# Kernel tuning notes

Hardware: AMD Instinct MI355X
Metric: run time of the kernel (lower is better)

Reference implementation:

```python
import jax, jax.numpy as jnp
import numpy as np

H = 16            # num heads
D_NOPE = 128
D_ROPE = 64
D_V = 128
Q_LORA = 1536
KV_LORA = 512
HIDDEN = 2048
EPS = 1e-6


def rmsnorm(x, w):
    xf = x.astype(jnp.float32)
    var = jnp.mean(xf * xf, axis=-1, keepdims=True)
    return (w * (xf * jax.lax.rsqrt(var + EPS))).astype(x.dtype)


def rope_interleaved(x, cos, sin):
    # x: [B,H,S,D]; cos,sin: [S,D] -> use even-index entries as the per-pair values
    B, nH, S, D = x.shape
    cv = cos[:, 0::2].astype(jnp.float32)[None, None]  # [1,1,S,D/2]
    sv = sin[:, 0::2].astype(jnp.float32)[None, None]
    xf = x.astype(jnp.float32).reshape(B, nH, S, D // 2, 2)
    xr, xi = xf[..., 0], xf[..., 1]
    out = jnp.stack([xr * cv - xi * sv, xr * sv + xi * cv], axis=-1)
    return out.reshape(B, nH, S, D).astype(x.dtype)


def setup_inputs() -> dict:
    key = jax.random.key(0)
    ks = jax.random.split(key, 9)
    B, S = 2, 2048
    std = 0.02
    return {
        "hidden_states": jax.random.normal(ks[0], (B, S, HIDDEN), jnp.float32),
        "cos": jax.random.uniform(ks[1], (S, D_ROPE), jnp.float32),
        "sin": jax.random.uniform(ks[2], (S, D_ROPE), jnp.float32),
        "q_a_w": jax.random.normal(ks[3], (HIDDEN, Q_LORA), jnp.float32) * std,
        "q_a_ln_w": jnp.ones((Q_LORA,), jnp.float32),
        "q_b_w": jax.random.normal(ks[4], (Q_LORA, H * (D_NOPE + D_ROPE)), jnp.float32) * std,
        "kv_a_w": jax.random.normal(ks[5], (HIDDEN, KV_LORA + D_ROPE), jnp.float32) * std,
        "kv_a_ln_w": jnp.ones((KV_LORA,), jnp.float32),
        "kv_b_w": jax.random.normal(ks[6], (KV_LORA, H * (D_NOPE + D_V)), jnp.float32) * std,
        "o_w": jax.random.normal(ks[7], (H * D_V, HIDDEN), jnp.float32) * std,
    }


def reference(hidden_states, cos, sin, q_a_w, q_a_ln_w, q_b_w, kv_a_w, kv_a_ln_w, kv_b_w, o_w):
    B, S, _ = hidden_states.shape
    scale = 1.0 / np.sqrt(D_NOPE + D_ROPE)

    # Q path: low-rank down-proj, RMSNorm, up-proj
    q = rmsnorm(hidden_states @ q_a_w, q_a_ln_w) @ q_b_w
    q = q.reshape(B, S, H, D_NOPE + D_ROPE).transpose(0, 2, 1, 3)  # [B,H,S,Dq]
    q_nope, q_rope = q[..., :D_NOPE], q[..., D_NOPE:]

    # KV path: compressed kv + shared rope key
    ckv = hidden_states @ kv_a_w  # [B,S,KV_LORA+D_ROPE]
    compressed_kv, k_rope = ckv[..., :KV_LORA], ckv[..., KV_LORA:]
    k_rope = jnp.broadcast_to(k_rope[:, None], (B, H, S, D_ROPE))
    kv = rmsnorm(compressed_kv, kv_a_ln_w) @ kv_b_w
    kv = kv.reshape(B, S, H, D_NOPE + D_V).transpose(0, 2, 1, 3)  # [B,H,S,Dk+Dv]
    k_nope, value = kv[..., :D_NOPE], kv[..., D_NOPE:]

    q_rope = rope_interleaved(q_rope, cos, sin)
    k_rope = rope_interleaved(k_rope, cos, sin)

    query = jnp.concatenate([q_nope, q_rope], axis=-1)  # [B,H,S,192]
    key = jnp.concatenate([k_nope, k_rope], axis=-1)

    attn = jnp.einsum("bhqd,bhkd->bhqk", query, key) * scale
    attn = jax.nn.softmax(attn.astype(jnp.float32), axis=-1).astype(query.dtype)
    out = jnp.einsum("bhqk,bhkd->bhqd", attn, value)  # [B,H,S,Dv]
    out = out.transpose(0, 2, 1, 3).reshape(B, S, H * D_V)
    return out @ o_w
```

## Files before the change

### kernel.cpp

```cpp
#include <hip/hip_runtime.h>

typedef unsigned short u16;
typedef __bf16 bf16x8 __attribute__((ext_vector_type(8)));
typedef float f32x4 __attribute__((ext_vector_type(4)));

#define S_ 2048

__device__ __forceinline__ u16 f2bf(float f) {
  union { float f; unsigned u; } v; v.f = f;
  unsigned r = v.u + 0x7fffu + ((v.u >> 16) & 1u);
  return (u16)(r >> 16);
}
__device__ __forceinline__ float bf2f(u16 h) {
  union { unsigned u; float f; } v; v.u = ((unsigned)h) << 16;
  return v.f;
}

__device__ __forceinline__ f32x4 mfma16(bf16x8 a, bf16x8 b, f32x4 c) {
  return __builtin_amdgcn_mfma_f32_16x16x32_bf16(a, b, c, 0, 0, 0);
}

__device__ __forceinline__ void async16(const void* g, void* l) {
  __builtin_amdgcn_global_load_lds((__attribute__((address_space(1))) void*)g,
                                   (__attribute__((address_space(3))) void*)l,
                                   16, 0, 0);
}

__global__ void cast_bf_k(const float* __restrict__ in, u16* __restrict__ out, int n) {
  int i = blockIdx.x * 256 + threadIdx.x;
  if (i < n) out[i] = f2bf(in[i]);
}

__global__ void transw_k(const float* __restrict__ W, u16* __restrict__ Wt,
                         int K, int N) {
  __shared__ float tile[32][33];
  int k0 = blockIdx.x * 32, n0 = blockIdx.y * 32;
  int tx = threadIdx.x, ty = threadIdx.y;
#pragma unroll
  for (int r = 0; r < 32; r += 8) {
    int n = n0 + tx;
    tile[ty + r][tx] = (n < N) ? W[(long)(k0 + ty + r) * N + n] : 0.f;
  }
  __syncthreads();
#pragma unroll
  for (int r = 0; r < 32; r += 8) {
    Wt[(long)(n0 + ty + r) * K + k0 + tx] = f2bf(tile[tx][ty + r]);
  }
}

template <typename OUT_T, bool ROPE>
__global__ __launch_bounds__(256)
void gemm_bt_k(const u16* __restrict__ A, const u16* __restrict__ Bt,
               OUT_T* __restrict__ C, int K, int Nc, int ldc,
               const float* __restrict__ cs, const float* __restrict__ sn) {
  __shared__ __align__(16) u16 sA[128 * 32];
  __shared__ __align__(16) u16 sB[128 * 32];
  int tid = threadIdx.x;
  int lane = tid & 63, w = tid >> 6;
  int wr = w >> 1, wc = w & 1;
  int l15 = lane & 15, quad = lane >> 4;
  long tm = (long)blockIdx.y * 128;
  long tn = (long)blockIdx.x * 128;
  const u16* Ab = A + tm * K;
  const u16* Bb = Bt + tn * K;
  f32x4 acc[4][4] = {};

  for (int k0 = 0; k0 < K; k0 += 32) {
#pragma unroll
    for (int it = 0; it < 2; ++it) {
      int c = tid + it * 256;
      int row = c >> 2, kc = c & 3;
      async16(Ab + (long)row * K + k0 + kc * 8, sA + c * 8);
      async16(Bb + (long)row * K + k0 + kc * 8, sB + c * 8);
    }
    __syncthreads();
    bf16x8 af[4], bfr[4];
#pragma unroll
    for (int i = 0; i < 4; ++i)
      af[i] = *(const bf16x8*)(sA + (wr * 64 + i * 16 + l15) * 32 + quad * 8);
#pragma unroll
    for (int j = 0; j < 4; ++j)
      bfr[j] = *(const bf16x8*)(sB + (wc * 64 + j * 16 + l15) * 32 + quad * 8);
#pragma unroll
    for (int i = 0; i < 4; ++i)
#pragma unroll
      for (int j = 0; j < 4; ++j)
        acc[i][j] = mfma16(af[i], bfr[j], acc[i][j]);
    __syncthreads();
  }
#pragma unroll
  for (int i = 0; i < 4; ++i) {
#pragma unroll
    for (int j = 0; j < 4; ++j) {
      int col = (int)tn + wc * 64 + j * 16 + l15;
      if (col < Nc) {
        bool ropeT = false;
        int fi = 0;
        if constexpr (ROPE) {
          int d = col % 192;
          ropeT = (d >= 128);
          fi = (d - 128) & ~1;
        }
#pragma unroll
        for (int r = 0; r < 4; ++r) {
          long row = tm + wr * 64 + i * 16 + quad * 4 + r;
          float v = acc[i][j][r];
          if constexpr (ROPE) {
            float partner = __shfl_xor(v, 1);
            if (ropeT) {
              int si = (int)row & (S_ - 1);
              float cv = cs[si * 64 + fi], sv = sn[si * 64 + fi];
              v = (l15 & 1) ? (partner * sv + v * cv)
                            : (v * cv - partner * sv);
            }
          }
          if constexpr (sizeof(OUT_T) == 2) C[row * ldc + col] = f2bf(v);
          else                              C[row * ldc + col] = v;
        }
      }
    }
  }
}

__global__ __launch_bounds__(256)
void rmsnorm_k(const float* __restrict__ in, int ld, int N,
               const float* __restrict__ w, u16* __restrict__ out, int ldo) {
  int row = blockIdx.x;
  const float* x = in + (long)row * ld;
  float ss = 0.f;
  for (int i = threadIdx.x; i < N; i += 256) { float v = x[i]; ss += v * v; }
#pragma unroll
  for (int off = 32; off; off >>= 1) ss += __shfl_down(ss, off);
  __shared__ float red[4];
  if ((threadIdx.x & 63) == 0) red[threadIdx.x >> 6] = ss;
  __syncthreads();
  float inv = rsqrtf((red[0] + red[1] + red[2] + red[3]) / N + 1e-6f);
  u16* o = out + (long)row * ldo;
  for (int i = threadIdx.x; i < N; i += 256) o[i] = f2bf(w[i] * x[i] * inv);
}

__global__ void krope_k(const float* __restrict__ src, int ld,
                        const float* __restrict__ cs, const float* __restrict__ sn,
                        u16* __restrict__ out) {
  int idx = blockIdx.x * 256 + threadIdx.x;
  int row = idx >> 5, i = idx & 31;
  int s = row & (S_ - 1);
  float xr = src[(long)row * ld + 2 * i];
  float xi = src[(long)row * ld + 2 * i + 1];
  float cv = cs[s * 64 + 2 * i], sv = sn[s * 64 + 2 * i];
  out[(long)row * 64 + 2 * i]     = f2bf(xr * cv - xi * sv);
  out[(long)row * 64 + 2 * i + 1] = f2bf(xr * sv + xi * cv);
}

__global__ void kswz_k(const u16* __restrict__ kvb, const u16* __restrict__ kr,
                       u16* __restrict__ kswz) {
  int tile = blockIdx.x;
  int bh = tile >> 5, kt = tile & 31;
  int b = bh >> 4, h = bh & 15;
  u16* dst = kswz + (long)tile * 12288;
#pragma unroll
  for (int i = 0; i < 6; ++i) {
    int c = threadIdx.x + i * 256;
    int frag = c >> 6, lane = c & 63;
    int kg = frag / 6, db = frag % 6;
    int key = kt * 64 + kg * 16 + (lane & 15);
    int d = db * 32 + (lane >> 4) * 8;
    const u16* src;
    if (d < 128) src = kvb + ((long)(b * S_ + key)) * 4096 + h * 256 + d;
    else         src = kr  + ((long)(b * S_ + key)) * 64 + (d - 128);
    *(f32x4*)(dst + c * 8) = *(const f32x4*)src;
  }
}

__global__ void vswz2_k(const u16* __restrict__ kvb, u16* __restrict__ vswz) {
  int tile = blockIdx.x;
  int bh = tile >> 5, kt = tile & 31;
  int b = bh >> 4, h = bh & 15;
  __shared__ __align__(16) u16 t[64 * 136];
  int tid = threadIdx.x;
#pragma unroll
  for (int i = 0; i < 4; ++i) {
    int c = tid + i * 256;
    int row = c >> 4, dc = (c & 15) * 8;
    *(f32x4*)(t + row * 136 + dc) =
        *(const f32x4*)(kvb + ((long)(b * S_ + kt * 64 + row)) * 4096 + h * 256 + 128 + dc);
  }
  __syncthreads();
  u16* dst = vswz + (long)tile * 8192;
#pragma unroll
  for (int i = 0; i < 4; ++i) {
    int c = tid + i * 256;
    int frag = c >> 6, lane = c & 63;
    int kq = frag >> 3, j = frag & 7;
    int d = j * 16 + (lane & 15);
    int keyl = kq * 32 + (lane >> 4) * 8;
    union { u16 v[8]; f32x4 q; } u;
#pragma unroll
    for (int e = 0; e < 8; ++e) u.v[e] = t[(keyl + e) * 136 + d];
    *(f32x4*)(dst + c * 8) = u.q;
  }
}

__global__ __launch_bounds__(256, 2)
void attn_k(const u16* __restrict__ qb, const u16* __restrict__ kswz,
            const u16* __restrict__ vswz, u16* __restrict__ attnO) {
  int bh = blockIdx.y, b = bh >> 4, h = bh & 15;
  int qt = blockIdx.x;
  int tid = threadIdx.x, lane = tid & 63, w = tid >> 6;
  int l15 = lane & 15, quad = lane >> 4;
  int qrow0 = qt * 128 + w * 32;

  __shared__ __align__(16) u16 sK[24 * 64 * 8];
  __shared__ __align__(16) u16 sV[16 * 64 * 8];
  __shared__ __align__(16) u16 pT[4][32 * 72];

  bf16x8 qf[2][6];
#pragma unroll
  for (int rg = 0; rg < 2; ++rg) {
    const u16* qp = qb + ((long)(b * S_ + qrow0 + rg * 16 + l15)) * 3072 + h * 192 + quad * 8;
#pragma unroll
    for (int kb = 0; kb < 6; ++kb) qf[rg][kb] = *(const bf16x8*)(qp + kb * 32);
  }

  f32x4 o[2][8] = {};
  float lsum[2][4] = {};
  u16* pw = pT[w];
  const float scale = 0.07216878364870322f;

#pragma unroll 1
  for (int kt = 0; kt < 32; ++kt) {
    const u16* Kt = kswz + ((long)bh * 32 + kt) * 12288;
    const u16* Vt = vswz + ((long)bh * 32 + kt) * 8192;
    __syncthreads();
#pragma unroll
    for (int i = 0; i < 6; ++i) {
      int c = tid + i * 256;
      async16(Kt + c * 8, sK + c * 8);
    }
#pragma unroll
    for (int i = 0; i < 4; ++i) {
      int c = tid + i * 256;
      async16(Vt + c * 8, sV + c * 8);
    }
    __syncthreads();

    f32x4 s[2][4] = {};
#pragma unroll
    for (int kg = 0; kg < 4; ++kg) {
#pragma unroll
      for (int db = 0; db < 6; ++db) {
        bf16x8 kf = *(const bf16x8*)(sK + ((kg * 6 + db) * 64 + lane) * 8);
        s[0][kg] = mfma16(qf[0][db], kf, s[0][kg]);
        s[1][kg] = mfma16(qf[1][db], kf, s[1][kg]);
      }
    }
#pragma unroll
    for (int rg = 0; rg < 2; ++rg) {
#pragma unroll
      for (int kg = 0; kg < 4; ++kg) {
#pragma unroll
        for (int r = 0; r < 4; ++r) {
          float p = __expf(s[rg][kg][r] * scale);
          lsum[rg][r] += p;
          pw[(rg * 16 + quad * 4 + r) * 72 + kg * 16 + l15] = f2bf(p);
        }
      }
    }
#pragma unroll
    for (int kq = 0; kq < 2; ++kq) {
      bf16x8 pf0 = *(const bf16x8*)(pw + (l15) * 72 + kq * 32 + quad * 8);
      bf16x8 pf1 = *(const bf16x8*)(pw + (16 + l15) * 72 + kq * 32 + quad * 8);
#pragma unroll
      for (int j = 0; j < 8; ++j) {
        bf16x8 vf = *(const bf16x8*)(sV + ((kq * 8 + j) * 64 + lane) * 8);
        o[0][j] = mfma16(pf0, vf, o[0][j]);
        o[1][j] = mfma16(pf1, vf, o[1][j]);
      }
    }
  }

  float inv[2][4];
#pragma unroll
  for (int rg = 0; rg < 2; ++rg)
#pragma unroll
    for (int r = 0; r < 4; ++r) {
      float s = lsum[rg][r];
#pragma unroll
      for (int off = 8; off; off >>= 1) s += __shfl_xor(s, off);
      inv[rg][r] = 1.f / s;
    }
#pragma unroll
  for (int rg = 0; rg < 2; ++rg) {
    u16* op = attnO + ((long)(b * S_ + qrow0 + rg * 16)) * 2048 + h * 128;
#pragma unroll
    for (int j = 0; j < 8; ++j)
#pragma unroll
      for (int r = 0; r < 4; ++r)
        op[(long)(quad * 4 + r) * 2048 + j * 16 + l15] = f2bf(o[rg][j][r] * inv[rg][r]);
  }
}

extern "C" void kernel_launch(void* const* d_in, const int* in_sizes, int n_in,
                              void* d_out, int out_size, void* d_ws, size_t ws_size,
                              hipStream_t stream) {
  const float* hs      = (const float*)d_in[0];
  const float* cosb    = (const float*)d_in[1];
  const float* sinb    = (const float*)d_in[2];
  const float* q_a_w   = (const float*)d_in[3];
  const float* q_a_ln  = (const float*)d_in[4];
  const float* q_b_w   = (const float*)d_in[5];
  const float* kv_a_w  = (const float*)d_in[6];
  const float* kv_a_ln = (const float*)d_in[7];
  const float* kv_b_w  = (const float*)d_in[8];
  const float* o_w     = (const float*)d_in[9];
  float* out = (float*)d_out;
  (void)in_sizes; (void)n_in; (void)out_size; (void)ws_size;

  char* p = (char*)d_ws;
  auto alloc = [&](size_t b) { char* r = p; p += (b + 255) & ~((size_t)255); return r; };
  u16*   hs_bf  = (u16*)  alloc((size_t)4096 * 2048 * 2);
  u16*   qakvT  = (u16*)  alloc((size_t)2176 * 2048 * 2);
  u16*   qbwT   = (u16*)  alloc((size_t)3072 * 1536 * 2);
  u16*   kvbwT  = (u16*)  alloc((size_t)4096 * 512  * 2);
  u16*   owT    = (u16*)  alloc((size_t)2048 * 2048 * 2);
  float* qa_ckv = (float*)alloc((size_t)4096 * 2176 * 4);
  u16*   qan    = (u16*)  alloc((size_t)4096 * 1536 * 2);
  u16*   ckvn   = (u16*)  alloc((size_t)4096 * 512  * 2);
  u16*   kr     = (u16*)  alloc((size_t)4096 * 64   * 2);
  u16*   qbuf   = (u16*)  alloc((size_t)4096 * 3072 * 2);
  u16*   kvbuf  = (u16*)  alloc((size_t)4096 * 4096 * 2);
  u16*   aO     = (u16*)  alloc((size_t)4096 * 2048 * 2);
  u16* kswz = (u16*)qa_ckv;
  u16* vswz = (u16*)hs_bf;

  dim3 tb(32, 8);
  cast_bf_k<<<32768, 256, 0, stream>>>(hs, hs_bf, 4096 * 2048);
  transw_k<<<dim3(64, 48),  tb, 0, stream>>>(q_a_w,  qakvT,                     2048, 1536);
  transw_k<<<dim3(64, 20),  tb, 0, stream>>>(kv_a_w, qakvT + (long)1536 * 2048, 2048, 576);
  transw_k<<<dim3(48, 96),  tb, 0, stream>>>(q_b_w,  qbwT,  1536, 3072);
  transw_k<<<dim3(16, 128), tb, 0, stream>>>(kv_b_w, kvbwT, 512,  4096);
  transw_k<<<dim3(64, 64),  tb, 0, stream>>>(o_w,    owT,   2048, 2048);

  gemm_bt_k<float, false><<<dim3(17, 32), 256, 0, stream>>>(
      hs_bf, qakvT, qa_ckv, 2048, 2176, 2176, nullptr, nullptr);
  rmsnorm_k<<<4096, 256, 0, stream>>>(qa_ckv,        2176, 1536, q_a_ln,  qan,  1536);
  rmsnorm_k<<<4096, 256, 0, stream>>>(qa_ckv + 1536, 2176, 512,  kv_a_ln, ckvn, 512);
  krope_k<<<512, 256, 0, stream>>>(qa_ckv + 2048, 2176, cosb, sinb, kr);
  gemm_bt_k<u16, true><<<dim3(24, 32), 256, 0, stream>>>(
      qan, qbwT, qbuf, 1536, 3072, 3072, cosb, sinb);
  gemm_bt_k<u16, false><<<dim3(32, 32), 256, 0, stream>>>(
      ckvn, kvbwT, kvbuf, 512, 4096, 4096, nullptr, nullptr);
  kswz_k<<<1024, 256, 0, stream>>>(kvbuf, kr, kswz);
  vswz2_k<<<1024, 256, 0, stream>>>(kvbuf, vswz);
  attn_k<<<dim3(16, 32), 256, 0, stream>>>(qbuf, kswz, vswz, aO);
  gemm_bt_k<float, false><<<dim3(16, 32), 256, 0, stream>>>(
      aO, owT, out, 2048, 2048, 2048, nullptr, nullptr);
}
```

Measured before the change: 518.5 us.

## Fuse KV up-projection with swizzled K/V layout writes, merge rmsnorms, vectorize cast

```diff
diff --git a/kernel.cpp b/kernel.cpp
--- a/kernel.cpp
+++ b/kernel.cpp
@@ -3,6 +3,7 @@
 typedef unsigned short u16;
 typedef __bf16 bf16x8 __attribute__((ext_vector_type(8)));
 typedef float f32x4 __attribute__((ext_vector_type(4)));
+typedef u16 u16x4 __attribute__((ext_vector_type(4)));
 
 #define S_ 2048
 
@@ -26,9 +27,15 @@
                                    16, 0, 0);
 }
 
-__global__ void cast_bf_k(const float* __restrict__ in, u16* __restrict__ out, int n) {
+__global__ void cast_bf8_k(const float* __restrict__ in, u16* __restrict__ out, int n8) {
   int i = blockIdx.x * 256 + threadIdx.x;
-  if (i < n) out[i] = f2bf(in[i]);
+  if (i < n8) {
+    f32x4 a = ((const f32x4*)in)[2 * i], b = ((const f32x4*)in)[2 * i + 1];
+    union { u16 v[8]; f32x4 q; } u;
+#pragma unroll
+    for (int e = 0; e < 4; ++e) { u.v[e] = f2bf(a[e]); u.v[4 + e] = f2bf(b[e]); }
+    ((f32x4*)out)[i] = u.q;
+  }
 }
 
 __global__ void transw_k(const float* __restrict__ W, u16* __restrict__ Wt,
@@ -123,10 +130,89 @@
 }
 
 __global__ __launch_bounds__(256)
-void rmsnorm_k(const float* __restrict__ in, int ld, int N,
-               const float* __restrict__ w, u16* __restrict__ out, int ldo) {
-  int row = blockIdx.x;
-  const float* x = in + (long)row * ld;
+void gemm_kvb_k(const u16* __restrict__ A, const u16* __restrict__ Bt,
+                u16* __restrict__ kswz, u16* __restrict__ vswz) {
+  const int K = 512;
+  __shared__ __align__(16) u16 sA[128 * 32];
+  __shared__ __align__(16) u16 sB[128 * 32];
+  int tid = threadIdx.x;
+  int lane = tid & 63, w = tid >> 6;
+  int wr = w >> 1, wc = w & 1;
+  int l15 = lane & 15, quad = lane >> 4;
+  long tm = (long)blockIdx.y * 128;
+  long tn = (long)blockIdx.x * 128;
+  const u16* Ab = A + tm * K;
+  const u16* Bb = Bt + tn * K;
+  f32x4 acc[4][4] = {};
+
+  for (int k0 = 0; k0 < K; k0 += 32) {
+#pragma unroll
+    for (int it = 0; it < 2; ++it) {
+      int c = tid + it * 256;
+      int row = c >> 2, kc = c & 3;
+      async16(Ab + (long)row * K + k0 + kc * 8, sA + c * 8);
+      async16(Bb + (long)row * K + k0 + kc * 8, sB + c * 8);
+    }
+    __syncthreads();
+    bf16x8 af[4], bfr[4];
+#pragma unroll
+    for (int i = 0; i < 4; ++i)
+      af[i] = *(const bf16x8*)(sA + (wr * 64 + i * 16 + l15) * 32 + quad * 8);
+#pragma unroll
+    for (int j = 0; j < 4; ++j)
+      bfr[j] = *(const bf16x8*)(sB + (wc * 64 + j * 16 + l15) * 32 + quad * 8);
+#pragma unroll
+    for (int i = 0; i < 4; ++i)
+#pragma unroll
+      for (int j = 0; j < 4; ++j)
+        acc[i][j] = mfma16(af[i], bfr[j], acc[i][j]);
+    __syncthreads();
+  }
+
+  int h = (int)(tn >> 8);
+  int b = (int)(tm >> 11);
+  int tile = (b * 16 + h) * 32 + (((int)tm & 2047) >> 6) + wr;
+  if ((tn & 255) == 0) {
+    u16* dst = kswz + (long)tile * 12288;
+#pragma unroll
+    for (int i = 0; i < 4; ++i) {
+#pragma unroll
+      for (int j = 0; j < 4; ++j) {
+        int frag = i * 6 + wc * 2 + (j >> 1);
+        int chunk = frag * 64 + ((j & 1) * 2 + (l15 >> 3)) * 16 + quad * 4;
+#pragma unroll
+        for (int r = 0; r < 4; ++r)
+          dst[(chunk + r) * 8 + (l15 & 7)] = f2bf(acc[i][j][r]);
+      }
+    }
+  } else {
+    u16* dst = vswz + (long)tile * 8192;
+#pragma unroll
+    for (int i = 0; i < 4; ++i) {
+      int laneHi = ((i & 1) * 2 + (quad >> 1)) << 4;
+      int kq = i >> 1;
+      int e0 = (quad & 1) * 4;
+#pragma unroll
+      for (int j = 0; j < 4; ++j) {
+        int frag = kq * 8 + wc * 4 + j;
+        u16x4 pk;
+#pragma unroll
+        for (int r = 0; r < 4; ++r) pk[r] = f2bf(acc[i][j][r]);
+        *(u16x4*)(dst + (frag * 64 + l15 + laneHi) * 8 + e0) = pk;
+      }
+    }
+  }
+}
+
+__global__ __launch_bounds__(256)
+void rmsnorm2_k(const float* __restrict__ qsrc, int ldq,
+                const float* __restrict__ kvsrc, int ldkv,
+                const float* __restrict__ wq, const float* __restrict__ wkv,
+                u16* __restrict__ qout, u16* __restrict__ kvout) {
+  int blk = blockIdx.x;
+  const float* x; const float* wt; u16* o; int N;
+  if (blk < 4096) { x = qsrc + (long)blk * ldq;  wt = wq;  o = qout + (long)blk * 1536;  N = 1536; }
+  else { blk -= 4096; x = kvsrc + (long)blk * ldkv; wt = wkv; o = kvout + (long)blk * 512; N = 512; }
   float ss = 0.f;
   for (int i = threadIdx.x; i < N; i += 256) { float v = x[i]; ss += v * v; }
 #pragma unroll
@@ -135,8 +221,7 @@
   if ((threadIdx.x & 63) == 0) red[threadIdx.x >> 6] = ss;
   __syncthreads();
   float inv = rsqrtf((red[0] + red[1] + red[2] + red[3]) / N + 1e-6f);
-  u16* o = out + (long)row * ldo;
-  for (int i = threadIdx.x; i < N; i += 256) o[i] = f2bf(w[i] * x[i] * inv);
+  for (int i = threadIdx.x; i < N; i += 256) o[i] = f2bf(wt[i] * x[i] * inv);
 }
 
 __global__ void krope_k(const float* __restrict__ src, int ld,
@@ -152,52 +237,21 @@
   out[(long)row * 64 + 2 * i + 1] = f2bf(xr * sv + xi * cv);
 }
 
-__global__ void kswz_k(const u16* __restrict__ kvb, const u16* __restrict__ kr,
-                       u16* __restrict__ kswz) {
+__global__ void krfill_k(const u16* __restrict__ kr, u16* __restrict__ kswz) {
   int tile = blockIdx.x;
   int bh = tile >> 5, kt = tile & 31;
-  int b = bh >> 4, h = bh & 15;
+  int b = bh >> 4;
   u16* dst = kswz + (long)tile * 12288;
 #pragma unroll
-  for (int i = 0; i < 6; ++i) {
-    int c = threadIdx.x + i * 256;
-    int frag = c >> 6, lane = c & 63;
-    int kg = frag / 6, db = frag % 6;
+  for (int it = 0; it < 2; ++it) {
+    int c = threadIdx.x + it * 256;
+    int lane = c & 63, fd = c >> 6;
+    int kg = fd >> 1, dbr = fd & 1;
     int key = kt * 64 + kg * 16 + (lane & 15);
-    int d = db * 32 + (lane >> 4) * 8;
-    const u16* src;
-    if (d < 128) src = kvb + ((long)(b * S_ + key)) * 4096 + h * 256 + d;
-    else         src = kr  + ((long)(b * S_ + key)) * 64 + (d - 128);
-    *(f32x4*)(dst + c * 8) = *(const f32x4*)src;
-  }
-}
-
-__global__ void vswz2_k(const u16* __restrict__ kvb, u16* __restrict__ vswz) {
-  int tile = blockIdx.x;
-  int bh = tile >> 5, kt = tile & 31;
-  int b = bh >> 4, h = bh & 15;
-  __shared__ __align__(16) u16 t[64 * 136];
-  int tid = threadIdx.x;
-#pragma unroll
-  for (int i = 0; i < 4; ++i) {
-    int c = tid + i * 256;
-    int row = c >> 4, dc = (c & 15) * 8;
-    *(f32x4*)(t + row * 136 + dc) =
-        *(const f32x4*)(kvb + ((long)(b * S_ + kt * 64 + row)) * 4096 + h * 256 + 128 + dc);
-  }
-  __syncthreads();
-  u16* dst = vswz + (long)tile * 8192;
-#pragma unroll
-  for (int i = 0; i < 4; ++i) {
-    int c = tid + i * 256;
-    int frag = c >> 6, lane = c & 63;
-    int kq = frag >> 3, j = frag & 7;
-    int d = j * 16 + (lane & 15);
-    int keyl = kq * 32 + (lane >> 4) * 8;
-    union { u16 v[8]; f32x4 q; } u;
-#pragma unroll
-    for (int e = 0; e < 8; ++e) u.v[e] = t[(keyl + e) * 136 + d];
-    *(f32x4*)(dst + c * 8) = u.q;
+    int doff = dbr * 32 + (lane >> 4) * 8;
+    int frag = kg * 6 + 4 + dbr;
+    *(f32x4*)(dst + (frag * 64 + lane) * 8) =
+        *(const f32x4*)(kr + ((long)(b * S_ + key)) * 64 + doff);
   }
 }
 
@@ -328,13 +382,12 @@
   u16*   ckvn   = (u16*)  alloc((size_t)4096 * 512  * 2);
   u16*   kr     = (u16*)  alloc((size_t)4096 * 64   * 2);
   u16*   qbuf   = (u16*)  alloc((size_t)4096 * 3072 * 2);
-  u16*   kvbuf  = (u16*)  alloc((size_t)4096 * 4096 * 2);
   u16*   aO     = (u16*)  alloc((size_t)4096 * 2048 * 2);
   u16* kswz = (u16*)qa_ckv;
   u16* vswz = (u16*)hs_bf;
 
   dim3 tb(32, 8);
-  cast_bf_k<<<32768, 256, 0, stream>>>(hs, hs_bf, 4096 * 2048);
+  cast_bf8_k<<<4096, 256, 0, stream>>>(hs, hs_bf, 4096 * 2048 / 8);
   transw_k<<<dim3(64, 48),  tb, 0, stream>>>(q_a_w,  qakvT,                     2048, 1536);
   transw_k<<<dim3(64, 20),  tb, 0, stream>>>(kv_a_w, qakvT + (long)1536 * 2048, 2048, 576);
   transw_k<<<dim3(48, 96),  tb, 0, stream>>>(q_b_w,  qbwT,  1536, 3072);
@@ -343,15 +396,13 @@
 
   gemm_bt_k<float, false><<<dim3(17, 32), 256, 0, stream>>>(
       hs_bf, qakvT, qa_ckv, 2048, 2176, 2176, nullptr, nullptr);
-  rmsnorm_k<<<4096, 256, 0, stream>>>(qa_ckv,        2176, 1536, q_a_ln,  qan,  1536);
-  rmsnorm_k<<<4096, 256, 0, stream>>>(qa_ckv + 1536, 2176, 512,  kv_a_ln, ckvn, 512);
+  rmsnorm2_k<<<8192, 256, 0, stream>>>(qa_ckv, 2176, qa_ckv + 1536, 2176,
+                                       q_a_ln, kv_a_ln, qan, ckvn);
   krope_k<<<512, 256, 0, stream>>>(qa_ckv + 2048, 2176, cosb, sinb, kr);
   gemm_bt_k<u16, true><<<dim3(24, 32), 256, 0, stream>>>(
       qan, qbwT, qbuf, 1536, 3072, 3072, cosb, sinb);
-  gemm_bt_k<u16, false><<<dim3(32, 32), 256, 0, stream>>>(
-      ckvn, kvbwT, kvbuf, 512, 4096, 4096, nullptr, nullptr);
-  kswz_k<<<1024, 256, 0, stream>>>(kvbuf, kr, kswz);
-  vswz2_k<<<1024, 256, 0, stream>>>(kvbuf, vswz);
+  gemm_kvb_k<<<dim3(32, 32), 256, 0, stream>>>(ckvn, kvbwT, kswz, vswz);
+  krfill_k<<<1024, 256, 0, stream>>>(kr, kswz);
   attn_k<<<dim3(16, 32), 256, 0, stream>>>(qbuf, kswz, vswz, aO);
   gemm_bt_k<float, false><<<dim3(16, 32), 256, 0, stream>>>(
       aO, owT, out, 2048, 2048, 2048, nullptr, nullptr);
```

After: 501.4 us. -3.3%, faster.
